# Performance work log

Hardware: AMD Instinct MI355X
Metric: run time of the kernel (lower is better)

Reference implementation:

```python
import jax, jax.numpy as jnp
import numpy as np

L = 32768      # sequence length
D_MODEL = 256  # input/output feature dim
D_HIDDEN = 256 # diagonal recurrent state dim
R_MIN, R_MAX, MAX_PHASE = 0.0, 1.0, 6.28


def setup_inputs() -> dict:
    key = jax.random.key(0)
    ks = jax.random.split(key, 8)
    inputs = jax.random.normal(ks[0], (L, D_MODEL), dtype=jnp.float32)
    # nu_init: log(-0.5*log(u*(r_max^2-r_min^2)+r_min^2))
    u1 = jax.random.uniform(ks[1], (D_HIDDEN,), dtype=jnp.float32)
    nu_log = jnp.log(-0.5 * jnp.log(u1 * (R_MAX**2 - R_MIN**2) + R_MIN**2))
    # theta_init: log(max_phase*u)
    u2 = jax.random.uniform(ks[2], (D_HIDDEN,), dtype=jnp.float32)
    theta_log = jnp.log(MAX_PHASE * u2)
    # gamma_log_init from (nu_log, theta_log)
    diag_lambda = jnp.exp(-jnp.exp(nu_log) + 1j * jnp.exp(theta_log))
    gamma_log = jnp.log(jnp.sqrt(1.0 - jnp.abs(diag_lambda) ** 2))
    bnorm = np.sqrt(2 * D_MODEL).astype(np.float32) if False else jnp.sqrt(2.0 * D_MODEL)
    cnorm = jnp.sqrt(2.0 * D_HIDDEN)
    B_re = jax.random.normal(ks[3], (D_HIDDEN, D_MODEL), dtype=jnp.float32) / bnorm
    B_im = jax.random.normal(ks[4], (D_HIDDEN, D_MODEL), dtype=jnp.float32) / bnorm
    C_re = jax.random.normal(ks[5], (D_MODEL, D_HIDDEN), dtype=jnp.float32) / cnorm
    C_im = jax.random.normal(ks[6], (D_MODEL, D_HIDDEN), dtype=jnp.float32) / cnorm
    D = jax.random.normal(ks[7], (D_MODEL,), dtype=jnp.float32)
    return {"inputs": inputs, "nu_log": nu_log, "theta_log": theta_log,
            "gamma_log": gamma_log, "B_re": B_re, "B_im": B_im,
            "C_re": C_re, "C_im": C_im, "D": D}


def _binop(q_i, q_j):
    # elementwise diagonal linear-recurrence combine
    A_i, b_i = q_i
    A_j, b_j = q_j
    return (A_j * A_i, A_j * b_i + b_j)


def reference(inputs, nu_log, theta_log, gamma_log, B_re, B_im, C_re, C_im, D):
    # h_{t+1} = lambda * h_t + B_norm x_{t+1};  y_t = Re[C h_t] + D * x_t
    diag_lambda = jnp.exp(-jnp.exp(nu_log) + 1j * jnp.exp(theta_log))  # (H,)
    B_norm = (B_re + 1j * B_im) * jnp.exp(gamma_log)[:, None]          # (H, M)
    C = C_re + 1j * C_im                                               # (M, H)
    Bu = inputs.astype(B_norm.dtype) @ B_norm.T                        # (L, H) complex
    Lam = jnp.broadcast_to(diag_lambda, (inputs.shape[0], diag_lambda.shape[0]))
    _, h = jax.lax.associative_scan(_binop, (Lam, Bu))                 # (L, H)
    return jnp.real(h @ C.T) + inputs * D                              # (L, M)
```

## Files before the change

kernel.cpp:

```cpp
#include <hip/hip_runtime.h>
#include <hip/hip_bf16.h>
#include <math.h>

#define LSEQ 32768
#define DMODEL 256
#define DHID 256
#define NCH 512
#define CHUNK 128
#define NCHUNKS (LSEQ / CHUNK)

typedef __bf16 bf16_t;
typedef _Float16 f16_t;
typedef __bf16 bf16x8 __attribute__((ext_vector_type(8)));
typedef float f32x4 __attribute__((ext_vector_type(4)));

__device__ __forceinline__ void async_load16(const void* g, void* l) {
  __builtin_amdgcn_global_load_lds((__attribute__((address_space(1))) void*)g,
                                   (__attribute__((address_space(3))) void*)l,
                                   16, 0, 0);
}

__device__ __forceinline__ float f16tof(unsigned int u) {
  return (float)__builtin_bit_cast(_Float16, (unsigned short)(u & 0xffffu));
}
__device__ __forceinline__ unsigned int fTobf(float f) {
  return (unsigned int)__builtin_bit_cast(unsigned short, (bf16_t)f);
}

__global__ void prep_all(const float* __restrict__ nu_log,
                         const float* __restrict__ theta_log,
                         const float* __restrict__ gamma_log,
                         const float* __restrict__ B_re, const float* __restrict__ B_im,
                         const float* __restrict__ C_re, const float* __restrict__ C_im,
                         float* __restrict__ lam, bf16_t* __restrict__ W1,
                         bf16_t* __restrict__ W2) {
  const int bid = blockIdx.x, tid = threadIdx.x;
  if (bid < 10) {
    int h = tid;
    if (h < DHID) {
      double nu = exp((double)nu_log[h]);
      double th = exp((double)theta_log[h]);
      int row; double n;
      if (bid == 0)      { row = 0; n = 1.0; }
      else if (bid == 1) { row = 2; n = 32.0; }
      else               { row = 4 + 2 * (bid - 2); n = 128.0 * (double)(1 << (bid - 2)); }
      double mag = exp(-n * nu);
      double ph  = fmod(n * th, 6.283185307179586);
      lam[row * DHID + h]       = (float)(mag * cos(ph));
      lam[(row + 1) * DHID + h] = (float)(mag * sin(ph));
    }
  } else if (bid < 522) {
    int n = bid - 10, k = tid, h = n >> 1;
    float g = expf(gamma_log[h]);
    float v = (((n & 1) == 0) ? B_re[h * DMODEL + k] : B_im[h * DMODEL + k]) * g;
    W1[n * DMODEL + k] = (bf16_t)v;
  } else {
    int idx = bid - 522;
    int m = idx >> 1, k = (idx & 1) * 256 + tid, h = k >> 1;
    float v = ((k & 1) == 0) ? C_re[m * DHID + h] : -C_im[m * DHID + h];
    W2[m * NCH + k] = (bf16_t)v;
  }
}

__global__ __launch_bounds__(512, 4) void gemm1_scan(
    const float* __restrict__ X, const bf16_t* __restrict__ Bw,
    f16_t* __restrict__ Bu, const float* __restrict__ lam,
    float* __restrict__ E) {
  __shared__ __align__(16) char smem[69632];
  char*  Bt = smem;
  float* Ep = (float*)(smem + 65536);

  const int tid = threadIdx.x;
  const int gx = blockIdx.x;
  const int c  = blockIdx.y;
  const int r0 = c * CHUNK;
  const int c0 = gx * 256;
  const int wave = tid >> 6, lane = tid & 63;
  const int wm = wave & 1, wn = wave >> 1;
  const int lrow = lane & 15, lk = lane >> 4;
  const int ra = tid >> 2, ka = (tid & 3) * 8;

  f32x4 acc[4][4] = {};

  {
    const float* xrow = X + (size_t)(r0 + ra) * DMODEL + ka;
    float4 a0 = ((const float4*)xrow)[0];
    float4 a1 = ((const float4*)xrow)[1];
    async_load16(Bw + (size_t)(c0 + ra) * DMODEL + ka, smem + 8192 + tid * 16);
    async_load16(Bw + (size_t)(c0 + 128 + ra) * DMODEL + ka, smem + 16384 + tid * 16);
    bf16x8 av = {(bf16_t)a0.x, (bf16_t)a0.y, (bf16_t)a0.z, (bf16_t)a0.w,
                 (bf16_t)a1.x, (bf16_t)a1.y, (bf16_t)a1.z, (bf16_t)a1.w};
    *(bf16x8*)(smem + ra * 64 + ka * 2) = av;
  }
  asm volatile("s_waitcnt vmcnt(0) lgkmcnt(0)" ::: "memory");
  __builtin_amdgcn_s_barrier();

#pragma unroll
  for (int t = 0; t < 8; ++t) {
    const int cur = t & 1, nxt = cur ^ 1;
    const char* Asc = smem + cur * 24576;
    const char* Bsc = smem + 8192 + cur * 24576;
    float4 a0, a1;
    if (t < 7) {
      const int k0n = (t + 1) * 32;
      const float* xrow = X + (size_t)(r0 + ra) * DMODEL + k0n + ka;
      a0 = ((const float4*)xrow)[0];
      a1 = ((const float4*)xrow)[1];
      async_load16(Bw + (size_t)(c0 + ra) * DMODEL + k0n + ka,
                   smem + 8192 + nxt * 24576 + tid * 16);
      async_load16(Bw + (size_t)(c0 + 128 + ra) * DMODEL + k0n + ka,
                   smem + 16384 + nxt * 24576 + tid * 16);
    }
    bf16x8 af[4], bfr[4];
#pragma unroll
    for (int i = 0; i < 4; ++i)
      af[i] = *(const bf16x8*)(Asc + (wm * 64 + i * 16 + lrow) * 64 + lk * 16);
#pragma unroll
    for (int j = 0; j < 4; ++j)
      bfr[j] = *(const bf16x8*)(Bsc + (wn * 64 + j * 16 + lrow) * 64 + lk * 16);
#pragma unroll
    for (int i = 0; i < 4; ++i)
#pragma unroll
      for (int j = 0; j < 4; ++j)
        acc[i][j] = __builtin_amdgcn_mfma_f32_16x16x32_bf16(af[i], bfr[j], acc[i][j], 0, 0, 0);
    if (t < 7) {
      bf16x8 av = {(bf16_t)a0.x, (bf16_t)a0.y, (bf16_t)a0.z, (bf16_t)a0.w,
                   (bf16_t)a1.x, (bf16_t)a1.y, (bf16_t)a1.z, (bf16_t)a1.w};
      *(bf16x8*)(smem + nxt * 24576 + ra * 64 + ka * 2) = av;
    }
    asm volatile("s_waitcnt vmcnt(0) lgkmcnt(0)" ::: "memory");
    __builtin_amdgcn_s_barrier();
  }

#pragma unroll
  for (int i = 0; i < 4; ++i)
#pragma unroll
    for (int r = 0; r < 4; ++r) {
      int row = wm * 64 + i * 16 + lk * 4 + r;
      int key = (row & 7) << 4;
#pragma unroll
      for (int j = 0; j < 4; ++j) {
        int col = wn * 64 + j * 16 + lrow;
        *(f16_t*)(Bt + row * 512 + ((col * 2) ^ key)) = (f16_t)acc[i][j][r];
      }
    }
  __syncthreads();

  char* dst = (char*)Bu + (size_t)r0 * 1024 + gx * 512;
#pragma unroll
  for (int it = 0; it < 8; ++it) {
    int idx = it * 512 + tid;
    int row = idx >> 5, off = (idx & 31) * 16;
    *(f32x4*)(dst + (size_t)row * 1024 + off) = *(const f32x4*)(Bt + row * 512 + off);
  }

  {
    int p = tid & 127, seg = tid >> 7;
    int h = gx * 128 + p;
    float lre = lam[h], lim = lam[DHID + h];
    float sre = 0.f, sim = 0.f;
    int cb = 4 * p;
#pragma unroll 4
    for (int t = 0; t < 32; ++t) {
      int row = seg * 32 + t;
      unsigned int w = *(const unsigned int*)(Bt + row * 512 + (cb ^ ((row & 7) << 4)));
      float bre = f16tof(w), bim = f16tof(w >> 16);
      float nre = fmaf(lre, sre, fmaf(-lim, sim, bre));
      float nim = fmaf(lre, sim, fmaf(lim, sre, bim));
      sre = nre; sim = nim;
    }
    Ep[seg * 256 + 2 * p]     = sre;
    Ep[seg * 256 + 2 * p + 1] = sim;
  }
  __syncthreads();
  if (tid < 128) {
    int p = tid, h = gx * 128 + p;
    float ar = lam[2 * DHID + h], ai = lam[3 * DHID + h];
    float er = Ep[2 * p], ei = Ep[2 * p + 1];
#pragma unroll
    for (int s = 1; s < 4; ++s) {
      float tr = fmaf(ar, er, fmaf(-ai, ei, Ep[s * 256 + 2 * p]));
      float ti = fmaf(ar, ei, fmaf(ai, er, Ep[s * 256 + 2 * p + 1]));
      er = tr; ei = ti;
    }
    E[(size_t)c * NCH + 2 * h]     = er;
    E[(size_t)c * NCH + 2 * h + 1] = ei;
  }
}

__global__ __launch_bounds__(1024) void scan_gemm2(
    const f16_t* __restrict__ Bu, const bf16_t* __restrict__ W2,
    const float* __restrict__ lam, const float* __restrict__ E,
    const float* __restrict__ X, const float* __restrict__ Dv,
    float* __restrict__ out) {
  __shared__ __align__(16) char smem[155648];
  char*   H  = smem;
  bf16_t* Bs = (bf16_t*)(smem + 131072);
  float*  LB = (float*)(smem + 131072);
  float*  Pp = (float*)(smem + 135168);
  float*  Tt = (float*)(smem + 147456);

  const int tid = threadIdx.x;
  const int c = (int)gridDim.x - 1 - (int)blockIdx.x;
  const int r0 = c * CHUNK;

  const char* src = (const char*)Bu + (size_t)r0 * 1024;
#pragma unroll
  for (int it = 0; it < 8; ++it)
    async_load16(src + it * 16384 + tid * 16, H + it * 16384 + tid * 16);

  const char* w2src = (const char*)W2 + (size_t)(tid >> 2) * (NCH * 2) + (tid & 3) * 16;
  f32x4 wreg[2];
  wreg[0] = *(const f32x4*)(w2src);

  if (tid < 512) {
    int p = tid & 255, half = tid >> 8;
    int m = c >> 1;
    int lo = half ? m : 0, end = half ? c : m;
    float aR = lam[4 * DHID + p], aI = lam[5 * DHID + p];
    float sr = 0.f, si = 0.f;
#pragma unroll 4
    for (int k = lo; k < end; ++k) {
      float2 e = *(const float2*)(E + (size_t)k * NCH + 2 * p);
      float nr = fmaf(aR, sr, fmaf(-aI, si, e.x));
      float ni = fmaf(aR, si, fmaf(aI, sr, e.y));
      sr = nr; si = ni;
    }
    LB[half * 512 + 2 * p]     = sr;
    LB[half * 512 + 2 * p + 1] = si;
  }
  __syncthreads();

  {
    int p = tid & 255, seg = tid >> 8;
    float lre = lam[p], lim = lam[DHID + p];
    float sre = 0.f, sim = 0.f;
    int cb = 4 * p;
#pragma unroll 4
    for (int t = 0; t < 32; ++t) {
      int row = seg * 32 + t;
      unsigned int w = *(const unsigned int*)(H + row * 1024 + (cb ^ ((row & 7) << 4)));
      float bre = f16tof(w), bim = f16tof(w >> 16);
      float nre = fmaf(lre, sre, fmaf(-lim, sim, bre));
      float nim = fmaf(lre, sim, fmaf(lim, sre, bim));
      sre = nre; sim = nim;
    }
    Pp[seg * 512 + 2 * p]     = sre;
    Pp[seg * 512 + 2 * p + 1] = sim;
  }
  __syncthreads();

  if (tid < 256) {
    int p = tid;
    int lenb = c - (c >> 1);
    float pr = 1.f, pi = 0.f;
#pragma unroll
    for (int j = 0; j < 8; ++j)
      if (lenb & (1 << j)) {
        float br = lam[(4 + 2 * j) * DHID + p], bi = lam[(5 + 2 * j) * DHID + p];
        float nr = pr * br - pi * bi, ni = pr * bi + pi * br;
        pr = nr; pi = ni;
      }
    float sar = LB[2 * p], sai = LB[2 * p + 1];
    float sbr = LB[512 + 2 * p], sbi = LB[512 + 2 * p + 1];
    float tr = fmaf(pr, sar, fmaf(-pi, sai, sbr));
    float ti = fmaf(pr, sai, fmaf(pi, sar, sbi));
    float l32r = lam[2 * DHID + p], l32i = lam[3 * DHID + p];
    Tt[2 * p] = tr; Tt[2 * p + 1] = ti;
#pragma unroll
    for (int s = 1; s < 4; ++s) {
      float pR = Pp[(s - 1) * 512 + 2 * p], pI = Pp[(s - 1) * 512 + 2 * p + 1];
      float nr = fmaf(l32r, tr, fmaf(-l32i, ti, pR));
      float ni = fmaf(l32r, ti, fmaf(l32i, tr, pI));
      tr = nr; ti = ni;
      Tt[s * 512 + 2 * p] = tr; Tt[s * 512 + 2 * p + 1] = ti;
    }
  }
  __syncthreads();

  {
    int p = tid & 255, seg = tid >> 8;
    float lre = lam[p], lim = lam[DHID + p];
    float sre = Tt[seg * 512 + 2 * p], sim = Tt[seg * 512 + 2 * p + 1];
    int cb = 4 * p;
#pragma unroll 4
    for (int t = 0; t < 32; ++t) {
      int row = seg * 32 + t;
      unsigned int* ptr = (unsigned int*)(H + row * 1024 + (cb ^ ((row & 7) << 4)));
      unsigned int w = *ptr;
      float bre = f16tof(w), bim = f16tof(w >> 16);
      float nre = fmaf(lre, sre, fmaf(-lim, sim, bre));
      float nim = fmaf(lre, sim, fmaf(lim, sre, bim));
      sre = nre; sim = nim;
      *ptr = (fTobf(sim) << 16) | fTobf(sre);
    }
  }
  __syncthreads();

  const int wave = tid >> 6, lane = tid & 63;
  const int wm = wave & 3, wn = wave >> 2;
  const int lrow = lane & 15, lk = lane >> 4;
  *(f32x4*)((char*)Bs + tid * 16) = wreg[0];
  wreg[1] = *(const f32x4*)(w2src + 64);
  asm volatile("s_waitcnt lgkmcnt(0)" ::: "memory");
  __builtin_amdgcn_s_barrier();

  f32x4 acc[2][4] = {};
#pragma unroll
  for (int t = 0; t < 16; ++t) {
    const int k0 = t * 32;
    bf16x8 af[2], bfr[4];
#pragma unroll
    for (int i = 0; i < 2; ++i) {
      int m = wm * 32 + i * 16 + lrow;
      af[i] = *(const bf16x8*)(H + m * 1024 + ((2 * k0 + lk * 16) ^ ((m & 7) << 4)));
    }
#pragma unroll
    for (int j = 0; j < 4; ++j)
      bfr[j] = *(const bf16x8*)(Bs + (wn * 64 + j * 16 + lrow) * 32 + lk * 8);
#pragma unroll
    for (int i = 0; i < 2; ++i)
#pragma unroll
      for (int j = 0; j < 4; ++j)
        acc[i][j] = __builtin_amdgcn_mfma_f32_16x16x32_bf16(af[i], bfr[j], acc[i][j], 0, 0, 0);
    if (t < 15) {
      __builtin_amdgcn_s_barrier();
      *(f32x4*)((char*)Bs + tid * 16) = wreg[(t + 1) & 1];
      if (t < 14) wreg[t & 1] = *(const f32x4*)(w2src + 64 * (t + 2));
      asm volatile("s_waitcnt lgkmcnt(0)" ::: "memory");
      __builtin_amdgcn_s_barrier();
    }
  }

#pragma unroll
  for (int i = 0; i < 2; ++i)
#pragma unroll
    for (int r = 0; r < 4; ++r) {
      int row = r0 + wm * 32 + i * 16 + lk * 4 + r;
#pragma unroll
      for (int j = 0; j < 4; ++j) {
        int col = wn * 64 + j * 16 + lrow;
        float v = acc[i][j][r] + X[(size_t)row * DMODEL + col] * Dv[col];
        out[(size_t)row * DMODEL + col] = v;
      }
    }
}

extern "C" void kernel_launch(void* const* d_in, const int* in_sizes, int n_in,
                              void* d_out, int out_size, void* d_ws, size_t ws_size,
                              hipStream_t stream) {
  const float* inputs    = (const float*)d_in[0];
  const float* nu_log    = (const float*)d_in[1];
  const float* theta_log = (const float*)d_in[2];
  const float* gamma_log = (const float*)d_in[3];
  const float* B_re      = (const float*)d_in[4];
  const float* B_im      = (const float*)d_in[5];
  const float* C_re      = (const float*)d_in[6];
  const float* C_im      = (const float*)d_in[7];
  const float* Dvec      = (const float*)d_in[8];
  float* out = (float*)d_out;

  char* w = (char*)d_ws;
  bf16_t* W1 = (bf16_t*)w; w += (size_t)NCH * DMODEL * 2;
  bf16_t* W2 = (bf16_t*)w; w += (size_t)DMODEL * NCH * 2;
  float* lam = (float*)w;  w += 24576;
  f16_t* Bu  = (f16_t*)w;  w += (size_t)LSEQ * NCH * 2;
  float* E   = (float*)w;  w += (size_t)NCHUNKS * NCH * 4;

  prep_all<<<1034, 256, 0, stream>>>(nu_log, theta_log, gamma_log,
                                     B_re, B_im, C_re, C_im,
                                     lam, W1, W2);
  gemm1_scan<<<dim3(2, NCHUNKS), 512, 0, stream>>>(inputs, W1, Bu, lam, E);
  scan_gemm2<<<NCHUNKS, 1024, 0, stream>>>(Bu, W2, lam, E, inputs, Dvec, out);
}
```

Baseline: 148.3 us.

## Triple-buffer GEMM1 K-loop with prefetch distance two

Converts the gemm1_scan K-loop from double buffering to triple buffering in shared memory, prefetching two K-steps ahead and waiting only on older async loads (vmcnt(2)). This is meant to hide global load latency of the X and B-weight tiles behind the MFMA work. It grows LDS use from 68 KB to 76 KB, which may reduce how many blocks fit per CU, and adds more vmcnt bookkeeping.

```diff
diff --git a/kernel.cpp b/kernel.cpp
--- a/kernel.cpp
+++ b/kernel.cpp
@@ -66,9 +66,9 @@
     const float* __restrict__ X, const bf16_t* __restrict__ Bw,
     f16_t* __restrict__ Bu, const float* __restrict__ lam,
     float* __restrict__ E) {
-  __shared__ __align__(16) char smem[69632];
+  __shared__ __align__(16) char smem[77824];
   char*  Bt = smem;
-  float* Ep = (float*)(smem + 65536);
+  float* Ep = (float*)(smem + 73728);
 
   const int tid = threadIdx.x;
   const int gx = blockIdx.x;
@@ -81,35 +81,41 @@
   const int ra = tid >> 2, ka = (tid & 3) * 8;
 
   f32x4 acc[4][4] = {};
+  const float*  xbase = X + (size_t)(r0 + ra) * DMODEL + ka;
+  const bf16_t* bw0   = Bw + (size_t)(c0 + ra) * DMODEL + ka;
+  const bf16_t* bw1   = Bw + (size_t)(c0 + 128 + ra) * DMODEL + ka;
 
   {
-    const float* xrow = X + (size_t)(r0 + ra) * DMODEL + ka;
-    float4 a0 = ((const float4*)xrow)[0];
-    float4 a1 = ((const float4*)xrow)[1];
-    async_load16(Bw + (size_t)(c0 + ra) * DMODEL + ka, smem + 8192 + tid * 16);
-    async_load16(Bw + (size_t)(c0 + 128 + ra) * DMODEL + ka, smem + 16384 + tid * 16);
-    bf16x8 av = {(bf16_t)a0.x, (bf16_t)a0.y, (bf16_t)a0.z, (bf16_t)a0.w,
-                 (bf16_t)a1.x, (bf16_t)a1.y, (bf16_t)a1.z, (bf16_t)a1.w};
-    *(bf16x8*)(smem + ra * 64 + ka * 2) = av;
-  }
-  asm volatile("s_waitcnt vmcnt(0) lgkmcnt(0)" ::: "memory");
+    float4 a00 = ((const float4*)xbase)[0];
+    float4 a01 = ((const float4*)xbase)[1];
+    float4 a10 = ((const float4*)(xbase + 32))[0];
+    float4 a11 = ((const float4*)(xbase + 32))[1];
+    async_load16(bw0, smem + 8192 + tid * 16);
+    async_load16(bw1, smem + 16384 + tid * 16);
+    async_load16(bw0 + 32, smem + 24576 + 8192 + tid * 16);
+    async_load16(bw1 + 32, smem + 24576 + 16384 + tid * 16);
+    bf16x8 av0 = {(bf16_t)a00.x, (bf16_t)a00.y, (bf16_t)a00.z, (bf16_t)a00.w,
+                  (bf16_t)a01.x, (bf16_t)a01.y, (bf16_t)a01.z, (bf16_t)a01.w};
+    *(bf16x8*)(smem + ra * 64 + ka * 2) = av0;
+    bf16x8 av1 = {(bf16_t)a10.x, (bf16_t)a10.y, (bf16_t)a10.z, (bf16_t)a10.w,
+                  (bf16_t)a11.x, (bf16_t)a11.y, (bf16_t)a11.z, (bf16_t)a11.w};
+    *(bf16x8*)(smem + 24576 + ra * 64 + ka * 2) = av1;
+  }
+  asm volatile("s_waitcnt vmcnt(2) lgkmcnt(0)" ::: "memory");
   __builtin_amdgcn_s_barrier();
 
 #pragma unroll
   for (int t = 0; t < 8; ++t) {
-    const int cur = t & 1, nxt = cur ^ 1;
+    const int cur = t % 3, nx2 = (t + 2) % 3;
     const char* Asc = smem + cur * 24576;
     const char* Bsc = smem + 8192 + cur * 24576;
     float4 a0, a1;
-    if (t < 7) {
-      const int k0n = (t + 1) * 32;
-      const float* xrow = X + (size_t)(r0 + ra) * DMODEL + k0n + ka;
-      a0 = ((const float4*)xrow)[0];
-      a1 = ((const float4*)xrow)[1];
-      async_load16(Bw + (size_t)(c0 + ra) * DMODEL + k0n + ka,
-                   smem + 8192 + nxt * 24576 + tid * 16);
-      async_load16(Bw + (size_t)(c0 + 128 + ra) * DMODEL + k0n + ka,
-                   smem + 16384 + nxt * 24576 + tid * 16);
+    if (t < 6) {
+      const int k0n = (t + 2) * 32;
+      a0 = ((const float4*)(xbase + k0n))[0];
+      a1 = ((const float4*)(xbase + k0n))[1];
+      async_load16(bw0 + k0n, smem + nx2 * 24576 + 8192 + tid * 16);
+      async_load16(bw1 + k0n, smem + nx2 * 24576 + 16384 + tid * 16);
     }
     bf16x8 af[4], bfr[4];
 #pragma unroll
@@ -123,12 +129,14 @@
 #pragma unroll
       for (int j = 0; j < 4; ++j)
         acc[i][j] = __builtin_amdgcn_mfma_f32_16x16x32_bf16(af[i], bfr[j], acc[i][j], 0, 0, 0);
-    if (t < 7) {
+    if (t < 6) {
       bf16x8 av = {(bf16_t)a0.x, (bf16_t)a0.y, (bf16_t)a0.z, (bf16_t)a0.w,
                    (bf16_t)a1.x, (bf16_t)a1.y, (bf16_t)a1.z, (bf16_t)a1.w};
-      *(bf16x8*)(smem + nxt * 24576 + ra * 64 + ka * 2) = av;
-    }
-    asm volatile("s_waitcnt vmcnt(0) lgkmcnt(0)" ::: "memory");
+      *(bf16x8*)(smem + nx2 * 24576 + ra * 64 + ka * 2) = av;
+      asm volatile("s_waitcnt vmcnt(2) lgkmcnt(0)" ::: "memory");
+    } else {
+      asm volatile("s_waitcnt vmcnt(0) lgkmcnt(0)" ::: "memory");
+    }
     __builtin_amdgcn_s_barrier();
   }
 
```

Result: slower. 155.0 us (+4.5%).
